# Kernel optimization log

Hardware: AMD Instinct MI355X
Metric: run time of the kernel (lower is better)

## Reference

```python
import jax, jax.numpy as jnp
import numpy as np
from jax import lax

EPS = 1e-10
BN_EPS = 1e-5
T = 0.1
K = 64
B, D, H, Z = 2048, 2048, 512, 500


def _bn(x, g, b):
    # training-mode BatchNorm1d: biased batch stats over axis 0
    mu = x.mean(axis=0)
    var = ((x - mu) ** 2).mean(axis=0)
    return g * (x - mu) / jnp.sqrt(var + BN_EPS) + b


def _leaky(x):
    return jnp.where(x >= 0, x, 0.01 * x)


def setup_inputs() -> dict:
    key = jax.random.key(0)
    ks = jax.random.split(key, 16)
    def lin(k, fan_in, shape):
        return jax.random.normal(k, shape, jnp.float32) / np.sqrt(fan_in)
    return {
        'x': jax.random.uniform(ks[0], (B, D), jnp.float32),
        'u_gumbel': jax.random.uniform(ks[1], (B, D), jnp.float32),
        'eps': jax.random.normal(ks[2], (B, Z), jnp.float32),
        'wc_w1': lin(ks[3], D, (D, H)), 'wc_b1': jnp.zeros((H,)),
        'wc_g': jnp.ones((H,)), 'wc_beta': jnp.zeros((H,)),
        'wc_w2': lin(ks[4], H, (H, D)), 'wc_b2': jnp.zeros((D,)),
        'enc_w1': lin(ks[5], D, (D, 2 * H)), 'enc_b1': jnp.zeros((2 * H,)),
        'enc_g1': jnp.ones((2 * H,)), 'enc_beta1': jnp.zeros((2 * H,)),
        'enc_w2': lin(ks[6], 2 * H, (2 * H, H)), 'enc_b2': jnp.zeros((H,)),
        'enc_g2': jnp.ones((H,)), 'enc_beta2': jnp.zeros((H,)),
        'enc_w3': lin(ks[7], H, (H, H)), 'enc_b3': jnp.zeros((H,)),
        'enc_g3': jnp.ones((H,)), 'enc_beta3': jnp.zeros((H,)),
        'fc21_w': lin(ks[8], H, (H, Z)), 'fc21_b': jnp.zeros((Z,)),
        'fc22_w': lin(ks[9], H, (H, Z)), 'fc22_b': jnp.zeros((Z,)),
        'fc3_w': lin(ks[10], Z, (Z, H)), 'fc3_b': jnp.zeros((H,)),
        'fc3_g': jnp.ones((H,)), 'fc3_beta': jnp.zeros((H,)),
        'fc4_w': lin(ks[11], H, (H, D)), 'fc4_b': jnp.zeros((D,)),
    }


def _sample_subset(w_logits, u):
    # gumbel_keys: w += log(-log(u')) with u' in (EPS, 1)
    u = (1.0 - EPS) * u + EPS
    w = w_logits + jnp.log(-jnp.log(u))

    def step(carry, _):
        w, onehot, acc = carry
        khot_mask = jnp.maximum(1.0 - onehot, EPS)
        w = w + jnp.log(khot_mask)
        onehot = jax.nn.softmax(w / T, axis=-1)
        return (w, onehot, acc + onehot), None

    init = (w, jnp.zeros_like(w), jnp.zeros_like(w))
    (_, _, khot), _ = lax.scan(step, init, None, length=K)
    return khot


def reference(x, u_gumbel, eps,
              wc_w1, wc_b1, wc_g, wc_beta, wc_w2, wc_b2,
              enc_w1, enc_b1, enc_g1, enc_beta1,
              enc_w2, enc_b2, enc_g2, enc_beta2,
              enc_w3, enc_b3, enc_g3, enc_beta3,
              fc21_w, fc21_b, fc22_w, fc22_b,
              fc3_w, fc3_b, fc3_g, fc3_beta, fc4_w, fc4_b):
    # weight_creator: Linear -> BN -> ReLU -> Linear
    h = jax.nn.relu(_bn(x @ wc_w1 + wc_b1, wc_g, wc_beta))
    w_logits = h @ wc_w2 + wc_b2
    khot = _sample_subset(w_logits, u_gumbel)  # [B, D]
    xm = x * khot
    h1 = _leaky(_bn(xm @ enc_w1 + enc_b1, enc_g1, enc_beta1))
    h1 = _leaky(_bn(h1 @ enc_w2 + enc_b2, enc_g2, enc_beta2))
    h1 = _leaky(_bn(h1 @ enc_w3 + enc_b3, enc_g3, enc_beta3))
    mu = h1 @ fc21_w + fc21_b
    logvar = h1 @ fc22_w + fc22_b
    z = mu + eps * jnp.exp(0.5 * logvar)
    hd = _leaky(_bn(z @ fc3_w + fc3_b, fc3_g, fc3_beta))
    mu_x = jax.nn.sigmoid(hd @ fc4_w + fc4_b)
    return (mu_x, mu, logvar)
```

## Files before the change

### kernel.cpp

```cpp
#include <hip/hip_runtime.h>
#include <hip/hip_bf16.h>
#include <math.h>

#define B_DIM 2048
#define D_DIM 2048
#define H_DIM 512
#define Z_DIM 500

#define ACT_NONE 0
#define ACT_RELU 1
#define ACT_SIGMOID 2
#define ACT_LEAKY 3

typedef __attribute__((ext_vector_type(8))) _Float16 f16x8;
typedef __attribute__((ext_vector_type(4))) _Float16 f16x4;
typedef __attribute__((ext_vector_type(4))) float f32x4;

template<int BM, int BN, int TERMS>
__global__ __launch_bounds__(256, 2) void gemm_f16(
    const _Float16* __restrict__ Ah_, const _Float16* __restrict__ Al_,
    const _Float16* __restrict__ Bh_, const _Float16* __restrict__ Bl_,
    const float* __restrict__ bias, float* __restrict__ C,
    float* __restrict__ part, int M, int N, int K, int act, int Kc)
{
    constexpr int LDK = 40;
    constexpr int NPL = (TERMS == 3) ? 2 : 1;
    constexpr int PSA = BM * LDK, PSB = BN * LDK;
    constexpr int BUF = NPL * (PSA + PSB);
    constexpr int MT = BM / 32, NT = BN / 32;
    constexpr int CA = BM / 64, CB = BN / 64;
    __shared__ _Float16 smem[2 * BUF];

    const int t = threadIdx.x, lane = t & 63, wv = t >> 6;
    const int wrow = wv >> 1, wcol = wv & 1;
    const int row0 = blockIdx.y * BM, col0 = blockIdx.x * BN;
    const int ks = blockIdx.z * Kc;
    const int nk = Kc >> 5;

    f16x8 rA[CA][NPL], rB[CB][NPL];

    auto gload = [&](int kt) {
        #pragma unroll
        for (int i = 0; i < CA; ++i) {
            int id = t + i * 256;
            int r = id >> 2, ko = (id & 3) * 8;
            size_t off = (size_t)(row0 + r) * K + kt + ko;
            rA[i][0] = *(const f16x8*)(Ah_ + off);
            if constexpr (TERMS == 3) rA[i][1] = *(const f16x8*)(Al_ + off);
        }
        #pragma unroll
        for (int i = 0; i < CB; ++i) {
            int id = t + i * 256;
            int r = id >> 2, ko = (id & 3) * 8;
            size_t off = (size_t)(col0 + r) * K + kt + ko;
            rB[i][0] = *(const f16x8*)(Bh_ + off);
            if constexpr (TERMS == 3) rB[i][1] = *(const f16x8*)(Bl_ + off);
        }
    };
    auto cstore = [&](int b) {
        _Float16* base = smem + b * BUF;
        #pragma unroll
        for (int i = 0; i < CA; ++i) {
            int id = t + i * 256;
            int r = id >> 2, ko = (id & 3) * 8;
            *(f16x8*)&base[r * LDK + ko] = rA[i][0];
            if constexpr (TERMS == 3) *(f16x8*)&base[PSA + r * LDK + ko] = rA[i][1];
        }
        _Float16* bb = base + NPL * PSA;
        #pragma unroll
        for (int i = 0; i < CB; ++i) {
            int id = t + i * 256;
            int r = id >> 2, ko = (id & 3) * 8;
            *(f16x8*)&bb[r * LDK + ko] = rB[i][0];
            if constexpr (TERMS == 3) *(f16x8*)&bb[PSB + r * LDK + ko] = rB[i][1];
        }
    };

    f32x4 acc[MT][NT];
    #pragma unroll
    for (int i = 0; i < MT; ++i)
        #pragma unroll
        for (int j = 0; j < NT; ++j) {
            f32x4 z = {0.f, 0.f, 0.f, 0.f};
            acc[i][j] = z;
        }

    const int q8 = (lane >> 4) * 8, fr = lane & 15;

    gload(ks);
    cstore(0);
    __syncthreads();

    for (int it = 0; it < nk; ++it) {
        int cur = it & 1;
        if (it + 1 < nk) gload(ks + (it + 1) * 32);

        const _Float16* A0 = smem + cur * BUF;
        const _Float16* A1 = A0 + PSA;
        const _Float16* B0 = A0 + NPL * PSA;
        const _Float16* B1 = B0 + PSB;
        f16x8 ah[MT], al[MT], bh[NT], bl[NT];
        #pragma unroll
        for (int i = 0; i < MT; ++i) {
            int r = wrow * (BM / 2) + i * 16 + fr;
            ah[i] = *(const f16x8*)&A0[r * LDK + q8];
            if constexpr (TERMS == 3) al[i] = *(const f16x8*)&A1[r * LDK + q8];
        }
        #pragma unroll
        for (int j = 0; j < NT; ++j) {
            int n = wcol * (BN / 2) + j * 16 + fr;
            bh[j] = *(const f16x8*)&B0[n * LDK + q8];
            if constexpr (TERMS == 3) bl[j] = *(const f16x8*)&B1[n * LDK + q8];
        }
        #pragma unroll
        for (int i = 0; i < MT; ++i)
            #pragma unroll
            for (int j = 0; j < NT; ++j) {
                acc[i][j] = __builtin_amdgcn_mfma_f32_16x16x32_f16(ah[i], bh[j], acc[i][j], 0, 0, 0);
                if constexpr (TERMS == 3) {
                    acc[i][j] = __builtin_amdgcn_mfma_f32_16x16x32_f16(ah[i], bl[j], acc[i][j], 0, 0, 0);
                    acc[i][j] = __builtin_amdgcn_mfma_f32_16x16x32_f16(al[i], bh[j], acc[i][j], 0, 0, 0);
                }
            }

        if (it + 1 < nk) cstore(cur ^ 1);
        __syncthreads();
    }

    const bool dopart = (gridDim.z > 1);
    float* dst = dopart ? (part + (size_t)blockIdx.z * M * N) : C;
    #pragma unroll
    for (int i = 0; i < MT; ++i) {
        int rbase = row0 + wrow * (BM / 2) + i * 16 + (lane >> 4) * 4;
        #pragma unroll
        for (int j = 0; j < NT; ++j) {
            int c = col0 + wcol * (BN / 2) + j * 16 + (lane & 15);
            if (c < N) {
                float b = dopart ? 0.f : bias[c];
                #pragma unroll
                for (int q = 0; q < 4; ++q) {
                    float v = acc[i][j][q] + b;
                    if (!dopart && act == ACT_SIGMOID)
                        v = 1.f / (1.f + __builtin_amdgcn_exp2f(-v * 1.44269504f));
                    dst[(size_t)(rbase + q) * N + c] = v;
                }
            }
        }
    }
}

__global__ __launch_bounds__(256) void cvt_split_x(
    const float* __restrict__ x, _Float16* __restrict__ xh,
    _Float16* __restrict__ xl, int n4)
{
    int i = blockIdx.x * 256 + threadIdx.x;
    if (i >= n4) return;
    float4 v = ((const float4*)x)[i];
    f16x4 h, l;
    h[0]=(_Float16)v.x; l[0]=(_Float16)(v.x-(float)h[0]);
    h[1]=(_Float16)v.y; l[1]=(_Float16)(v.y-(float)h[1]);
    h[2]=(_Float16)v.z; l[2]=(_Float16)(v.z-(float)h[2]);
    h[3]=(_Float16)v.w; l[3]=(_Float16)(v.w-(float)h[3]);
    ((f16x4*)xh)[i] = h;
    ((f16x4*)xl)[i] = l;
}

__global__ __launch_bounds__(256) void cvt_w_t(
    const float* __restrict__ in, _Float16* __restrict__ outh,
    _Float16* __restrict__ outl, int K, int N, int Kp)
{
    __shared__ float tile[32][33];
    const int t = threadIdx.x;
    const int tk0 = blockIdx.x * 32, tn0 = blockIdx.y * 32;
    const int lx = t & 31, ly = t >> 5;
    #pragma unroll
    for (int r = 0; r < 4; ++r) {
        int k = tk0 + ly + r * 8, n = tn0 + lx;
        tile[ly + r * 8][lx] = (k < K && n < N) ? in[(size_t)k * N + n] : 0.f;
    }
    __syncthreads();
    #pragma unroll
    for (int r = 0; r < 4; ++r) {
        int n = tn0 + ly + r * 8, k = tk0 + lx;
        float v = tile[lx][ly + r * 8];
        _Float16 h = (_Float16)v;
        outh[(size_t)n * Kp + k] = h;
        if (outl) outl[(size_t)n * Kp + k] = (_Float16)(v - (float)h);
    }
}

__global__ __launch_bounds__(256) void reduce_bias(
    const float* __restrict__ part, int S, int MN, int N,
    const float* __restrict__ bias, float* __restrict__ C, int act)
{
    int i = blockIdx.x * 256 + threadIdx.x;
    if (i >= MN) return;
    float s = bias[i % N];
    for (int k = 0; k < S; ++k) s += part[(size_t)k * MN + i];
    if (act == ACT_SIGMOID) s = 1.f / (1.f + __builtin_amdgcn_exp2f(-s * 1.44269504f));
    C[i] = s;
}

__global__ __launch_bounds__(256) void colstats_partial(
    const float* __restrict__ Y, float* __restrict__ part,
    int Brows, int N, int rowsPerBlock)
{
    const int t = threadIdx.x;
    const int col = blockIdx.x * 64 + (t & 63);
    const int g = blockIdx.y;
    const int r0 = g * rowsPerBlock;
    const int r1 = min(r0 + rowsPerBlock, Brows);
    float s = 0.f, s2 = 0.f;
    for (int r = r0 + (t >> 6); r < r1; r += 4) {
        float v = Y[(size_t)r * N + col];
        s += v;
        s2 += v * v;
    }
    __shared__ float ss[4][64], ss2[4][64];
    ss[t >> 6][t & 63] = s;
    ss2[t >> 6][t & 63] = s2;
    __syncthreads();
    if (t < 64) {
        s  = ss[0][t] + ss[1][t] + ss[2][t] + ss[3][t];
        s2 = ss2[0][t] + ss2[1][t] + ss2[2][t] + ss2[3][t];
        float* p = part + ((size_t)g * N + col) * 2;
        p[0] = s;
        p[1] = s2;
    }
}

__global__ __launch_bounds__(256) void colstats_final(
    const float* __restrict__ part, int G, int N, int Brows,
    const float* __restrict__ gamma, const float* __restrict__ beta,
    float* __restrict__ scale, float* __restrict__ shift)
{
    int c = blockIdx.x * 256 + threadIdx.x;
    if (c >= N) return;
    float s = 0.f, s2 = 0.f;
    for (int g = 0; g < G; ++g) {
        s  += part[((size_t)g * N + c) * 2];
        s2 += part[((size_t)g * N + c) * 2 + 1];
    }
    float invB = 1.f / (float)Brows;
    float mean = s * invB;
    float var  = s2 * invB - mean * mean;
    float rstd = rsqrtf(var + 1e-5f);
    float sc = gamma[c] * rstd;
    scale[c] = sc;
    shift[c] = beta[c] - mean * sc;
}

__global__ __launch_bounds__(256) void bn_apply_f16(
    const float* __restrict__ Y, const float* __restrict__ scale,
    const float* __restrict__ shift, _Float16* __restrict__ oh,
    _Float16* __restrict__ ol, int total, int N, int act)
{
    int idx = blockIdx.x * 256 + threadIdx.x;
    int i4 = idx * 4;
    if (i4 >= total) return;
    float4 y = *(const float4*)(Y + i4);
    int c = i4 % N;
    float4 sc = *(const float4*)(scale + c);
    float4 sh = *(const float4*)(shift + c);
    float r[4];
    r[0] = y.x * sc.x + sh.x;
    r[1] = y.y * sc.y + sh.y;
    r[2] = y.z * sc.z + sh.z;
    r[3] = y.w * sc.w + sh.w;
    #pragma unroll
    for (int q = 0; q < 4; ++q) {
        if (act == ACT_RELU) r[q] = fmaxf(r[q], 0.f);
        else if (act == ACT_LEAKY) r[q] = (r[q] >= 0.f) ? r[q] : 0.01f * r[q];
    }
    f16x4 h;
    #pragma unroll
    for (int q = 0; q < 4; ++q) h[q] = (_Float16)r[q];
    ((f16x4*)oh)[idx] = h;
    if (ol) {
        f16x4 l;
        #pragma unroll
        for (int q = 0; q < 4; ++q) l[q] = (_Float16)(r[q] - (float)h[q]);
        ((f16x4*)ol)[idx] = l;
    }
}

__global__ __launch_bounds__(256) void gumbel_scan(
    const float* __restrict__ WLg, const float* __restrict__ U,
    const float* __restrict__ X, _Float16* __restrict__ XM)
{
    const int row = blockIdx.x;
    const int t = threadIdx.x, wv = t >> 6, lane = t & 63;
    const float* wrow = WLg + (size_t)row * D_DIM;
    const float* urow = U + (size_t)row * D_DIM;
    const float* xrow = X + (size_t)row * D_DIM;
    _Float16* xmrow = XM + (size_t)row * D_DIM;

    const float L2E = 1.4426950408889634f;
    const float LOG2LN2 = -0.5287663729448977f;

    __shared__ float sW[2][4], sS[2][4];

    float W[8], e[8], acc[8];
    #pragma unroll
    for (int j = 0; j < 8; ++j) {
        int c = t + j * 256;
        float u = fmaf(urow[c], 1.0f - 1e-10f, 1e-10f);
        float tl = -__builtin_amdgcn_logf(u);
        float w2 = fmaf(wrow[c], L2E, __builtin_amdgcn_logf(tl) + LOG2LN2);
        W[j] = __builtin_amdgcn_exp2f(w2);
        e[j] = 0.f;
        acc[j] = 0.f;
    }
    float inv = 0.f;

    for (int it = 0; it < 64; ++it) {
        const int p = it & 1;
        float lm = 0.f;
        #pragma unroll
        for (int j = 0; j < 8; ++j) {
            acc[j] = fmaf(e[j], inv, acc[j]);
            float msk = fmaxf(fmaf(-e[j], inv, 1.0f), 1e-10f);
            W[j] *= msk;
            lm = fmaxf(lm, W[j]);
        }
        #pragma unroll
        for (int off = 32; off; off >>= 1)
            lm = fmaxf(lm, __shfl_xor(lm, off));
        if (lane == 0) sW[p][wv] = lm;
        __syncthreads();
        float Wm = fmaxf(fmaxf(sW[p][0], sW[p][1]), fmaxf(sW[p][2], sW[p][3]));
        float rm = 1.0f / Wm;
        float s = 0.f;
        #pragma unroll
        for (int j = 0; j < 8; ++j) {
            float r1 = W[j] * rm;
            float r2 = r1 * r1;
            float r4 = r2 * r2;
            float r5 = r4 * r1;
            float ee = r5 * r5;
            e[j] = ee;
            s += ee;
        }
        #pragma unroll
        for (int off = 32; off; off >>= 1)
            s += __shfl_xor(s, off);
        if (lane == 0) sS[p][wv] = s;
        __syncthreads();
        s = (sS[p][0] + sS[p][1]) + (sS[p][2] + sS[p][3]);
        inv = 1.0f / s;
    }

    #pragma unroll
    for (int j = 0; j < 8; ++j) {
        int c = t + j * 256;
        float a = fmaf(e[j], inv, acc[j]);
        xmrow[c] = (_Float16)(xrow[c] * a);
    }
}

__global__ __launch_bounds__(256) void z_kernel16(
    const float* __restrict__ mu, const float* __restrict__ lv,
    const float* __restrict__ eps, _Float16* __restrict__ zb, int n4)
{
    int i = blockIdx.x * 256 + threadIdx.x;
    if (i >= n4) return;
    int f = i * 4;
    int row = f / Z_DIM, col = f - row * Z_DIM;
    float4 m = *(const float4*)(mu + f);
    float4 l = *(const float4*)(lv + f);
    float4 e = *(const float4*)(eps + f);
    const float HL2E = 0.7213475204444817f;
    f16x4 r;
    r[0] = (_Float16)(m.x + e.x * __builtin_amdgcn_exp2f(l.x * HL2E));
    r[1] = (_Float16)(m.y + e.y * __builtin_amdgcn_exp2f(l.y * HL2E));
    r[2] = (_Float16)(m.z + e.z * __builtin_amdgcn_exp2f(l.z * HL2E));
    r[3] = (_Float16)(m.w + e.w * __builtin_amdgcn_exp2f(l.w * HL2E));
    *(f16x4*)(zb + (size_t)row * 512 + col) = r;
}

extern "C" void kernel_launch(void* const* d_in, const int* in_sizes, int n_in,
                              void* d_out, int out_size, void* d_ws, size_t ws_size,
                              hipStream_t stream) {
    const float* x        = (const float*)d_in[0];
    const float* u_gumbel = (const float*)d_in[1];
    const float* eps      = (const float*)d_in[2];
    const float* wc_w1    = (const float*)d_in[3];
    const float* wc_b1    = (const float*)d_in[4];
    const float* wc_g     = (const float*)d_in[5];
    const float* wc_beta  = (const float*)d_in[6];
    const float* wc_w2    = (const float*)d_in[7];
    const float* wc_b2    = (const float*)d_in[8];
    const float* enc_w1   = (const float*)d_in[9];
    const float* enc_b1   = (const float*)d_in[10];
    const float* enc_g1   = (const float*)d_in[11];
    const float* enc_beta1= (const float*)d_in[12];
    const float* enc_w2   = (const float*)d_in[13];
    const float* enc_b2   = (const float*)d_in[14];
    const float* enc_g2   = (const float*)d_in[15];
    const float* enc_beta2= (const float*)d_in[16];
    const float* enc_w3   = (const float*)d_in[17];
    const float* enc_b3   = (const float*)d_in[18];
    const float* enc_g3   = (const float*)d_in[19];
    const float* enc_beta3= (const float*)d_in[20];
    const float* fc21_w   = (const float*)d_in[21];
    const float* fc21_b   = (const float*)d_in[22];
    const float* fc22_w   = (const float*)d_in[23];
    const float* fc22_b   = (const float*)d_in[24];
    const float* fc3_w    = (const float*)d_in[25];
    const float* fc3_b    = (const float*)d_in[26];
    const float* fc3_g    = (const float*)d_in[27];
    const float* fc3_beta = (const float*)d_in[28];
    const float* fc4_w    = (const float*)d_in[29];
    const float* fc4_b    = (const float*)d_in[30];

    float* out   = (float*)d_out;
    float* mu_x  = out;
    float* mu    = out + (size_t)B_DIM * D_DIM;
    float* lv    = mu + (size_t)B_DIM * Z_DIM;

    const size_t F1M = 1u << 20;
    float* wsf = (float*)d_ws;
    float*     P_WL  = wsf;
    _Float16*  xh    = (_Float16*)(wsf + 4 * F1M);
    _Float16*  xl    = (_Float16*)(wsf + 6 * F1M);
    _Float16*  xm16  = (_Float16*)(wsf + 4 * F1M);
    float*     Yb    = wsf + 6 * F1M;
    _Float16*  a2    = (_Float16*)(wsf + 8 * F1M);
    _Float16*  a3    = (_Float16*)(wsf + 9 * F1M);
    _Float16*  a4    = (_Float16*)(wsf + 9 * F1M + F1M / 2);
    _Float16*  zb16  = (_Float16*)(wsf + 10 * F1M);
    _Float16*  a5    = (_Float16*)(wsf + 10 * F1M + F1M / 2);
    float*     Hbuf  = wsf + 11 * F1M;
    _Float16*  Hh    = (_Float16*)(wsf + 12 * F1M);
    _Float16*  Hl    = (_Float16*)(wsf + 12 * F1M + F1M / 2);
    _Float16*  w1th  = (_Float16*)(wsf + 13 * F1M);
    _Float16*  w1tl  = (_Float16*)(wsf + 13 * F1M + F1M / 2);
    _Float16*  w2th  = (_Float16*)(wsf + 14 * F1M);
    _Float16*  w2tl  = (_Float16*)(wsf + 14 * F1M + F1M / 2);
    _Float16*  e1t   = (_Float16*)(wsf + 15 * F1M);
    _Float16*  e2t   = (_Float16*)(wsf + 16 * F1M);
    _Float16*  e3t   = (_Float16*)(wsf + 16 * F1M + F1M / 4);
    _Float16*  f21t  = (_Float16*)(wsf + 16 * F1M + 3 * (F1M / 8));
    _Float16*  f22t  = (_Float16*)(wsf + 16 * F1M + 4 * (F1M / 8));
    _Float16*  f3t   = (_Float16*)(wsf + 16 * F1M + 5 * (F1M / 8));
    _Float16*  f4t   = (_Float16*)(wsf + 16 * F1M + 6 * (F1M / 8));
    float*     bnp   = wsf + 17 * F1M + F1M / 4;
    float*     scale = bnp + 16384;
    float*     shift = scale + 2048;

    const int G = 8;

    auto gemm3 = [&](const _Float16* Ah, const _Float16* Al,
                     const _Float16* Bh, const _Float16* Bl,
                     const float* b, float* C, float* part,
                     int N, int K, int SK) {
        dim3 grid((N + 63) / 64, B_DIM / 128, SK);
        gemm_f16<128, 64, 3><<<grid, 256, 0, stream>>>(Ah, Al, Bh, Bl, b, C, part,
                                                       B_DIM, N, K, ACT_NONE, K / SK);
    };
    auto gemm1 = [&](const _Float16* Ah, const _Float16* Bh,
                     const float* b, float* C, float* part,
                     int N, int K, int act, int SK) {
        dim3 grid((N + 63) / 64, B_DIM / 128, SK);
        gemm_f16<128, 64, 1><<<grid, 256, 0, stream>>>(Ah, nullptr, Bh, nullptr, b, C,
                                                       part, B_DIM, N, K, act, K / SK);
    };
    auto reduceK = [&](const float* part, int S, int N, const float* b, float* C) {
        int MN = B_DIM * N;
        reduce_bias<<<(MN + 255) / 256, 256, 0, stream>>>(part, S, MN, N, b, C, ACT_NONE);
    };
    auto bn = [&](const float* Y, const float* g_, const float* b_,
                  _Float16* oh, _Float16* ol, int N, int act) {
        dim3 gp(N / 64, G);
        colstats_partial<<<gp, 256, 0, stream>>>(Y, bnp, B_DIM, N, B_DIM / G);
        colstats_final<<<(N + 255) / 256, 256, 0, stream>>>(bnp, G, N, B_DIM, g_, b_, scale, shift);
        int total = B_DIM * N;
        bn_apply_f16<<<(total / 4 + 255) / 256, 256, 0, stream>>>(Y, scale, shift, oh, ol, total, N, act);
    };
    auto cvtw = [&](const float* in, _Float16* oh, _Float16* ol, int K, int N, int Kp, int Np) {
        dim3 grid(Kp / 32, Np / 32);
        cvt_w_t<<<grid, 256, 0, stream>>>(in, oh, ol, K, N, Kp);
    };

    cvt_split_x<<<4096, 256, 0, stream>>>(x, xh, xl, B_DIM * D_DIM / 4);
    cvtw(wc_w1, w1th, w1tl, 2048, 512, 2048, 512);
    cvtw(wc_w2, w2th, w2tl, 512, 2048, 512, 2048);
    cvtw(enc_w1, e1t, nullptr, 2048, 1024, 2048, 1024);
    cvtw(enc_w2, e2t, nullptr, 1024, 512, 1024, 512);
    cvtw(enc_w3, e3t, nullptr, 512, 512, 512, 512);
    cvtw(fc21_w, f21t, nullptr, 512, 500, 512, 512);
    cvtw(fc22_w, f22t, nullptr, 512, 500, 512, 512);
    cvtw(fc3_w, f3t, nullptr, 500, 512, 512, 512);
    cvtw(fc4_w, f4t, nullptr, 512, 2048, 512, 2048);

    gemm3(xh, xl, w1th, w1tl, nullptr, nullptr, P_WL, 512, 2048, 4);
    reduceK(P_WL, 4, 512, wc_b1, Hbuf);
    bn(Hbuf, wc_g, wc_beta, Hh, Hl, 512, ACT_RELU);
    gemm3(Hh, Hl, w2th, w2tl, wc_b2, P_WL, nullptr, 2048, 512, 1);

    gumbel_scan<<<B_DIM, 256, 0, stream>>>(P_WL, u_gumbel, x, xm16);

    gemm1(xm16, e1t, nullptr, nullptr, P_WL, 1024, 2048, ACT_NONE, 2);
    reduceK(P_WL, 2, 1024, enc_b1, Yb);
    bn(Yb, enc_g1, enc_beta1, a2, nullptr, 1024, ACT_LEAKY);
    gemm1(a2, e2t, nullptr, nullptr, P_WL, 512, 1024, ACT_NONE, 4);
    reduceK(P_WL, 4, 512, enc_b2, Yb);
    bn(Yb, enc_g2, enc_beta2, a3, nullptr, 512, ACT_LEAKY);
    gemm1(a3, e3t, nullptr, nullptr, P_WL, 512, 512, ACT_NONE, 4);
    reduceK(P_WL, 4, 512, enc_b3, Yb);
    bn(Yb, enc_g3, enc_beta3, a4, nullptr, 512, ACT_LEAKY);

    gemm1(a4, f21t, nullptr, nullptr, P_WL, 500, 512, ACT_NONE, 4);
    reduceK(P_WL, 4, 500, fc21_b, mu);
    gemm1(a4, f22t, nullptr, nullptr, P_WL, 500, 512, ACT_NONE, 4);
    reduceK(P_WL, 4, 500, fc22_b, lv);

    hipMemsetAsync(zb16, 0, (size_t)B_DIM * 512 * sizeof(_Float16), stream);
    int n4 = B_DIM * Z_DIM / 4;
    z_kernel16<<<(n4 + 255) / 256, 256, 0, stream>>>(mu, lv, eps, zb16, n4);

    gemm1(zb16, f3t, nullptr, nullptr, P_WL, 512, 512, ACT_NONE, 4);
    reduceK(P_WL, 4, 512, fc3_b, Yb);
    bn(Yb, fc3_g, fc3_beta, a5, nullptr, 512, ACT_LEAKY);
    gemm1(a5, f4t, fc4_b, mu_x, nullptr, 2048, 512, ACT_SIGMOID, 1);
}
```

Before: 465.2 us.

## Merge gumbel scan reductions into one barrier per iteration using stale max

The 64-step softmax scan in gumbel_scan now runs one combined max+sum block reduction per iteration instead of two. It normalises by the previous iteration's max, which is valid because the mask only ever shrinks W, so the ratio stays at or below one. The loop also uses packed f32x2 arithmetic, hardware rcp, and vectorised 8-wide loads and stores per thread. The cost is that the exponent is computed against a stale max, so there is a small underflow or precision risk, and the initial max needs an extra reduction.

```diff
diff --git a/kernel.cpp b/kernel.cpp
--- a/kernel.cpp
+++ b/kernel.cpp
@@ -15,6 +15,7 @@
 typedef __attribute__((ext_vector_type(8))) _Float16 f16x8;
 typedef __attribute__((ext_vector_type(4))) _Float16 f16x4;
 typedef __attribute__((ext_vector_type(4))) float f32x4;
+typedef __attribute__((ext_vector_type(2))) float f32x2;
 
 template<int BM, int BN, int TERMS>
 __global__ __launch_bounds__(256, 2) void gemm_f16(
@@ -290,71 +291,111 @@
 {
     const int row = blockIdx.x;
     const int t = threadIdx.x, wv = t >> 6, lane = t & 63;
-    const float* wrow = WLg + (size_t)row * D_DIM;
-    const float* urow = U + (size_t)row * D_DIM;
-    const float* xrow = X + (size_t)row * D_DIM;
-    _Float16* xmrow = XM + (size_t)row * D_DIM;
+    const float* wrow = WLg + (size_t)row * D_DIM + 8 * t;
+    const float* urow = U + (size_t)row * D_DIM + 8 * t;
+    const float* xrow = X + (size_t)row * D_DIM + 8 * t;
+    _Float16* xmrow = XM + (size_t)row * D_DIM + 8 * t;
 
     const float L2E = 1.4426950408889634f;
     const float LOG2LN2 = -0.5287663729448977f;
 
-    __shared__ float sW[2][4], sS[2][4];
-
-    float W[8], e[8], acc[8];
-    #pragma unroll
-    for (int j = 0; j < 8; ++j) {
-        int c = t + j * 256;
-        float u = fmaf(urow[c], 1.0f - 1e-10f, 1e-10f);
+    __shared__ f32x2 sLS[2][4];
+    __shared__ float sM0[4];
+
+    f32x2 W2[4], e2[4], acc2[4];
+
+    auto mkW = [&](float wl, float uu) -> float {
+        float u = fmaf(uu, 1.0f - 1e-10f, 1e-10f);
         float tl = -__builtin_amdgcn_logf(u);
-        float w2 = fmaf(wrow[c], L2E, __builtin_amdgcn_logf(tl) + LOG2LN2);
-        W[j] = __builtin_amdgcn_exp2f(w2);
-        e[j] = 0.f;
-        acc[j] = 0.f;
-    }
+        return __builtin_amdgcn_exp2f(fmaf(wl, L2E, __builtin_amdgcn_logf(tl) + LOG2LN2));
+    };
+
+    {
+        float4 ua = *(const float4*)urow, ub = *(const float4*)(urow + 4);
+        float4 wa = *(const float4*)wrow, wb = *(const float4*)(wrow + 4);
+        W2[0] = f32x2{mkW(wa.x, ua.x), mkW(wa.y, ua.y)};
+        W2[1] = f32x2{mkW(wa.z, ua.z), mkW(wa.w, ua.w)};
+        W2[2] = f32x2{mkW(wb.x, ub.x), mkW(wb.y, ub.y)};
+        W2[3] = f32x2{mkW(wb.z, ub.z), mkW(wb.w, ub.w)};
+    }
+    #pragma unroll
+    for (int j = 0; j < 4; ++j) {
+        e2[j] = f32x2{0.f, 0.f};
+        acc2[j] = f32x2{0.f, 0.f};
+    }
+
+    float m;
+    {
+        f32x2 lv = f32x2{0.f, 0.f};
+        #pragma unroll
+        for (int j = 0; j < 4; ++j) {
+            lv.x = fmaxf(lv.x, W2[j].x);
+            lv.y = fmaxf(lv.y, W2[j].y);
+        }
+        float lm = fmaxf(lv.x, lv.y);
+        #pragma unroll
+        for (int off = 32; off; off >>= 1)
+            lm = fmaxf(lm, __shfl_xor(lm, off));
+        if (lane == 0) sM0[wv] = lm;
+        __syncthreads();
+        m = fmaxf(fmaxf(sM0[0], sM0[1]), fmaxf(sM0[2], sM0[3]));
+    }
+
     float inv = 0.f;
-
     for (int it = 0; it < 64; ++it) {
         const int p = it & 1;
-        float lm = 0.f;
-        #pragma unroll
-        for (int j = 0; j < 8; ++j) {
-            acc[j] = fmaf(e[j], inv, acc[j]);
-            float msk = fmaxf(fmaf(-e[j], inv, 1.0f), 1e-10f);
-            W[j] *= msk;
-            lm = fmaxf(lm, W[j]);
-        }
-        #pragma unroll
-        for (int off = 32; off; off >>= 1)
+        const float rm = __builtin_amdgcn_rcpf(m);
+        f32x2 lmv = f32x2{0.f, 0.f}, sv = f32x2{0.f, 0.f};
+        #pragma unroll
+        for (int j = 0; j < 4; ++j) {
+            f32x2 oh = e2[j] * inv;
+            acc2[j] += oh;
+            f32x2 msk = 1.0f - oh;
+            msk.x = fmaxf(msk.x, 1e-10f);
+            msk.y = fmaxf(msk.y, 1e-10f);
+            f32x2 Wn = W2[j] * msk;
+            W2[j] = Wn;
+            f32x2 r = Wn * rm;
+            f32x2 q2 = r * r;
+            f32x2 q4 = q2 * q2;
+            f32x2 q8 = q4 * q4;
+            f32x2 ee = q8 * q2;
+            e2[j] = ee;
+            sv += ee;
+            lmv.x = fmaxf(lmv.x, Wn.x);
+            lmv.y = fmaxf(lmv.y, Wn.y);
+        }
+        float lm = fmaxf(lmv.x, lmv.y);
+        float s = sv.x + sv.y;
+        #pragma unroll
+        for (int off = 32; off; off >>= 1) {
             lm = fmaxf(lm, __shfl_xor(lm, off));
-        if (lane == 0) sW[p][wv] = lm;
+            s += __shfl_xor(s, off);
+        }
+        if (lane == 0) sLS[p][wv] = f32x2{lm, s};
         __syncthreads();
-        float Wm = fmaxf(fmaxf(sW[p][0], sW[p][1]), fmaxf(sW[p][2], sW[p][3]));
-        float rm = 1.0f / Wm;
-        float s = 0.f;
-        #pragma unroll
-        for (int j = 0; j < 8; ++j) {
-            float r1 = W[j] * rm;
-            float r2 = r1 * r1;
-            float r4 = r2 * r2;
-            float r5 = r4 * r1;
-            float ee = r5 * r5;
-            e[j] = ee;
-            s += ee;
-        }
-        #pragma unroll
-        for (int off = 32; off; off >>= 1)
-            s += __shfl_xor(s, off);
-        if (lane == 0) sS[p][wv] = s;
-        __syncthreads();
-        s = (sS[p][0] + sS[p][1]) + (sS[p][2] + sS[p][3]);
-        inv = 1.0f / s;
-    }
-
-    #pragma unroll
-    for (int j = 0; j < 8; ++j) {
-        int c = t + j * 256;
-        float a = fmaf(e[j], inv, acc[j]);
-        xmrow[c] = (_Float16)(xrow[c] * a);
+        f32x2 r0 = sLS[p][0], r1 = sLS[p][1], r2 = sLS[p][2], r3 = sLS[p][3];
+        m = fmaxf(fmaxf(r0.x, r1.x), fmaxf(r2.x, r3.x));
+        float st = (r0.y + r1.y) + (r2.y + r3.y);
+        inv = __builtin_amdgcn_rcpf(st);
+    }
+
+    {
+        float4 xa = *(const float4*)xrow, xb = *(const float4*)(xrow + 4);
+        f32x2 a0 = acc2[0] + e2[0] * inv;
+        f32x2 a1 = acc2[1] + e2[1] * inv;
+        f32x2 a2 = acc2[2] + e2[2] * inv;
+        f32x2 a3 = acc2[3] + e2[3] * inv;
+        f16x8 o;
+        o[0] = (_Float16)(xa.x * a0.x);
+        o[1] = (_Float16)(xa.y * a0.y);
+        o[2] = (_Float16)(xa.z * a1.x);
+        o[3] = (_Float16)(xa.w * a1.y);
+        o[4] = (_Float16)(xb.x * a2.x);
+        o[5] = (_Float16)(xb.y * a2.y);
+        o[6] = (_Float16)(xb.z * a3.x);
+        o[7] = (_Float16)(xb.w * a3.y);
+        *(f16x8*)xmrow = o;
     }
 }
 
```

Result: faster. 455.4 us (-2.1%).

## Fuse split-K reduce into BN stats and make gumbel scan one row per wave

Applied to the files above, without the earlier changes.

Replaces the separate split-K reduce_bias plus colstats_partial pair with a single reduce_stats kernel that sums partials, adds bias, writes Y and accumulates column stats, using 64 row groups instead of 8. Rewrites gumbel_scan so each wavefront owns a full row (32 elements per lane, vectorised loads and stores), which removes the block-level __syncthreads and shared-memory reductions. The per-step max renormalisation now refreshes only every 4 iterations, with the other steps reusing a stale max. This trades exact per-step max scaling for fewer reductions, with some overflow or precision risk in the x^10 power, and uses more registers per thread.

```diff
diff --git a/kernel.cpp b/kernel.cpp
--- a/kernel.cpp
+++ b/kernel.cpp
@@ -15,6 +15,10 @@
 typedef __attribute__((ext_vector_type(8))) _Float16 f16x8;
 typedef __attribute__((ext_vector_type(4))) _Float16 f16x4;
 typedef __attribute__((ext_vector_type(4))) float f32x4;
+
+__device__ __forceinline__ float rfl(float x) {
+    return __uint_as_float(__builtin_amdgcn_readfirstlane(__float_as_uint(x)));
+}
 
 template<int BM, int BN, int TERMS>
 __global__ __launch_bounds__(256, 2) void gemm_f16(
@@ -201,18 +205,23 @@
     C[i] = s;
 }
 
-__global__ __launch_bounds__(256) void colstats_partial(
-    const float* __restrict__ Y, float* __restrict__ part,
-    int Brows, int N, int rowsPerBlock)
+__global__ __launch_bounds__(256) void reduce_stats(
+    const float* __restrict__ part, int S, int Brows, int N, int rowsPerBlock,
+    const float* __restrict__ bias, float* __restrict__ Y,
+    float* __restrict__ statp)
 {
     const int t = threadIdx.x;
     const int col = blockIdx.x * 64 + (t & 63);
     const int g = blockIdx.y;
     const int r0 = g * rowsPerBlock;
     const int r1 = min(r0 + rowsPerBlock, Brows);
+    const size_t MN = (size_t)Brows * N;
+    const float b = bias[col];
     float s = 0.f, s2 = 0.f;
     for (int r = r0 + (t >> 6); r < r1; r += 4) {
-        float v = Y[(size_t)r * N + col];
+        float v = b;
+        for (int k = 0; k < S; ++k) v += part[k * MN + (size_t)r * N + col];
+        Y[(size_t)r * N + col] = v;
         s += v;
         s2 += v * v;
     }
@@ -223,7 +232,7 @@
     if (t < 64) {
         s  = ss[0][t] + ss[1][t] + ss[2][t] + ss[3][t];
         s2 = ss2[0][t] + ss2[1][t] + ss2[2][t] + ss2[3][t];
-        float* p = part + ((size_t)g * N + col) * 2;
+        float* p = statp + ((size_t)g * N + col) * 2;
         p[0] = s;
         p[1] = s2;
     }
@@ -288,8 +297,8 @@
     const float* __restrict__ WLg, const float* __restrict__ U,
     const float* __restrict__ X, _Float16* __restrict__ XM)
 {
-    const int row = blockIdx.x;
-    const int t = threadIdx.x, wv = t >> 6, lane = t & 63;
+    const int wv = threadIdx.x >> 6, lane = threadIdx.x & 63;
+    const int row = blockIdx.x * 4 + wv;
     const float* wrow = WLg + (size_t)row * D_DIM;
     const float* urow = U + (size_t)row * D_DIM;
     const float* xrow = X + (size_t)row * D_DIM;
@@ -298,63 +307,80 @@
     const float L2E = 1.4426950408889634f;
     const float LOG2LN2 = -0.5287663729448977f;
 
-    __shared__ float sW[2][4], sS[2][4];
-
-    float W[8], e[8], acc[8];
+    float W[32], acc[32];
+
+    auto mkW = [&](float wl, float uu) -> float {
+        float u = fmaf(uu, 1.0f - 1e-10f, 1e-10f);
+        float tl = -__builtin_amdgcn_logf(u);
+        return __builtin_amdgcn_exp2f(fmaf(wl, L2E, __builtin_amdgcn_logf(tl) + LOG2LN2));
+    };
+
     #pragma unroll
     for (int j = 0; j < 8; ++j) {
-        int c = t + j * 256;
-        float u = fmaf(urow[c], 1.0f - 1e-10f, 1e-10f);
-        float tl = -__builtin_amdgcn_logf(u);
-        float w2 = fmaf(wrow[c], L2E, __builtin_amdgcn_logf(tl) + LOG2LN2);
-        W[j] = __builtin_amdgcn_exp2f(w2);
-        e[j] = 0.f;
-        acc[j] = 0.f;
-    }
-    float inv = 0.f;
+        float4 u4 = *(const float4*)(urow + j * 256 + lane * 4);
+        float4 w4 = *(const float4*)(wrow + j * 256 + lane * 4);
+        W[4*j  ] = mkW(w4.x, u4.x);
+        W[4*j+1] = mkW(w4.y, u4.y);
+        W[4*j+2] = mkW(w4.z, u4.z);
+        W[4*j+3] = mkW(w4.w, u4.w);
+        acc[4*j] = 0.f; acc[4*j+1] = 0.f; acc[4*j+2] = 0.f; acc[4*j+3] = 0.f;
+    }
+
+    float rm_s;
+    {
+        float lm = 0.f;
+        #pragma unroll
+        for (int j = 0; j < 32; ++j) lm = fmaxf(lm, W[j]);
+        #pragma unroll
+        for (int off = 32; off; off >>= 1)
+            lm = fmaxf(lm, __shfl_xor(lm, off));
+        rm_s = rfl(__builtin_amdgcn_rcpf(lm));
+    }
 
     for (int it = 0; it < 64; ++it) {
-        const int p = it & 1;
+        float e[32];
+        float s = 0.f;
+        #pragma unroll
+        for (int j = 0; j < 32; ++j) {
+            float r1 = W[j] * rm_s;
+            float q2 = r1 * r1;
+            float q4 = q2 * q2;
+            float q8 = q4 * q4;
+            float ee = q8 * q2;
+            e[j] = ee;
+            s += ee;
+        }
+        #pragma unroll
+        for (int off = 32; off; off >>= 1)
+            s += __shfl_xor(s, off);
+        float inv = rfl(__builtin_amdgcn_rcpf(s));
+
+        const bool refresh = ((it & 3) == 3);
         float lm = 0.f;
         #pragma unroll
-        for (int j = 0; j < 8; ++j) {
+        for (int j = 0; j < 32; ++j) {
             acc[j] = fmaf(e[j], inv, acc[j]);
             float msk = fmaxf(fmaf(-e[j], inv, 1.0f), 1e-10f);
             W[j] *= msk;
-            lm = fmaxf(lm, W[j]);
-        }
-        #pragma unroll
-        for (int off = 32; off; off >>= 1)
-            lm = fmaxf(lm, __shfl_xor(lm, off));
-        if (lane == 0) sW[p][wv] = lm;
-        __syncthreads();
-        float Wm = fmaxf(fmaxf(sW[p][0], sW[p][1]), fmaxf(sW[p][2], sW[p][3]));
-        float rm = 1.0f / Wm;
-        float s = 0.f;
-        #pragma unroll
-        for (int j = 0; j < 8; ++j) {
-            float r1 = W[j] * rm;
-            float r2 = r1 * r1;
-            float r4 = r2 * r2;
-            float r5 = r4 * r1;
-            float ee = r5 * r5;
-            e[j] = ee;
-            s += ee;
-        }
-        #pragma unroll
-        for (int off = 32; off; off >>= 1)
-            s += __shfl_xor(s, off);
-        if (lane == 0) sS[p][wv] = s;
-        __syncthreads();
-        s = (sS[p][0] + sS[p][1]) + (sS[p][2] + sS[p][3]);
-        inv = 1.0f / s;
+            if (refresh) lm = fmaxf(lm, W[j]);
+        }
+        if (refresh) {
+            #pragma unroll
+            for (int off = 32; off; off >>= 1)
+                lm = fmaxf(lm, __shfl_xor(lm, off));
+            rm_s = rfl(__builtin_amdgcn_rcpf(lm));
+        }
     }
 
     #pragma unroll
     for (int j = 0; j < 8; ++j) {
-        int c = t + j * 256;
-        float a = fmaf(e[j], inv, acc[j]);
-        xmrow[c] = (_Float16)(xrow[c] * a);
+        float4 x4 = *(const float4*)(xrow + j * 256 + lane * 4);
+        f16x4 o;
+        o[0] = (_Float16)(x4.x * acc[4*j  ]);
+        o[1] = (_Float16)(x4.y * acc[4*j+1]);
+        o[2] = (_Float16)(x4.z * acc[4*j+2]);
+        o[3] = (_Float16)(x4.w * acc[4*j+3]);
+        *(f16x4*)(xmrow + j * 256 + lane * 4) = o;
     }
 }
 
@@ -445,10 +471,10 @@
     _Float16*  f3t   = (_Float16*)(wsf + 16 * F1M + 5 * (F1M / 8));
     _Float16*  f4t   = (_Float16*)(wsf + 16 * F1M + 6 * (F1M / 8));
     float*     bnp   = wsf + 17 * F1M + F1M / 4;
-    float*     scale = bnp + 16384;
+    float*     scale = bnp + 131072;
     float*     shift = scale + 2048;
 
-    const int G = 8;
+    const int G = 64;
 
     auto gemm3 = [&](const _Float16* Ah, const _Float16* Al,
                      const _Float16* Bh, const _Float16* Bl,
@@ -469,11 +495,12 @@
         int MN = B_DIM * N;
         reduce_bias<<<(MN + 255) / 256, 256, 0, stream>>>(part, S, MN, N, b, C, ACT_NONE);
     };
-    auto bn = [&](const float* Y, const float* g_, const float* b_,
-                  _Float16* oh, _Float16* ol, int N, int act) {
+    auto bnFromParts = [&](const float* part, int S, const float* b,
+                           const float* g_, const float* beta_,
+                           float* Y, _Float16* oh, _Float16* ol, int N, int act) {
         dim3 gp(N / 64, G);
-        colstats_partial<<<gp, 256, 0, stream>>>(Y, bnp, B_DIM, N, B_DIM / G);
-        colstats_final<<<(N + 255) / 256, 256, 0, stream>>>(bnp, G, N, B_DIM, g_, b_, scale, shift);
+        reduce_stats<<<gp, 256, 0, stream>>>(part, S, B_DIM, N, B_DIM / G, b, Y, bnp);
+        colstats_final<<<(N + 255) / 256, 256, 0, stream>>>(bnp, G, N, B_DIM, g_, beta_, scale, shift);
         int total = B_DIM * N;
         bn_apply_f16<<<(total / 4 + 255) / 256, 256, 0, stream>>>(Y, scale, shift, oh, ol, total, N, act);
     };
@@ -494,21 +521,17 @@
     cvtw(fc4_w, f4t, nullptr, 512, 2048, 512, 2048);
 
     gemm3(xh, xl, w1th, w1tl, nullptr, nullptr, P_WL, 512, 2048, 4);
-    reduceK(P_WL, 4, 512, wc_b1, Hbuf);
-    bn(Hbuf, wc_g, wc_beta, Hh, Hl, 512, ACT_RELU);
+    bnFromParts(P_WL, 4, wc_b1, wc_g, wc_beta, Hbuf, Hh, Hl, 512, ACT_RELU);
     gemm3(Hh, Hl, w2th, w2tl, wc_b2, P_WL, nullptr, 2048, 512, 1);
 
-    gumbel_scan<<<B_DIM, 256, 0, stream>>>(P_WL, u_gumbel, x, xm16);
+    gumbel_scan<<<B_DIM / 4, 256, 0, stream>>>(P_WL, u_gumbel, x, xm16);
 
     gemm1(xm16, e1t, nullptr, nullptr, P_WL, 1024, 2048, ACT_NONE, 2);
-    reduceK(P_WL, 2, 1024, enc_b1, Yb);
-    bn(Yb, enc_g1, enc_beta1, a2, nullptr, 1024, ACT_LEAKY);
+    bnFromParts(P_WL, 2, enc_b1, enc_g1, enc_beta1, Yb, a2, nullptr, 1024, ACT_LEAKY);
     gemm1(a2, e2t, nullptr, nullptr, P_WL, 512, 1024, ACT_NONE, 4);
-    reduceK(P_WL, 4, 512, enc_b2, Yb);
-    bn(Yb, enc_g2, enc_beta2, a3, nullptr, 512, ACT_LEAKY);
+    bnFromParts(P_WL, 4, enc_b2, enc_g2, enc_beta2, Yb, a3, nullptr, 512, ACT_LEAKY);
     gemm1(a3, e3t, nullptr, nullptr, P_WL, 512, 512, ACT_NONE, 4);
-    reduceK(P_WL, 4, 512, enc_b3, Yb);
-    bn(Yb, enc_g3, enc_beta3, a4, nullptr, 512, ACT_LEAKY);
+    bnFromParts(P_WL, 4, enc_b3, enc_g3, enc_beta3, Yb, a4, nullptr, 512, ACT_LEAKY);
 
     gemm1(a4, f21t, nullptr, nullptr, P_WL, 500, 512, ACT_NONE, 4);
     reduceK(P_WL, 4, 500, fc21_b, mu);
@@ -520,7 +543,6 @@
     z_kernel16<<<(n4 + 255) / 256, 256, 0, stream>>>(mu, lv, eps, zb16, n4);
 
     gemm1(zb16, f3t, nullptr, nullptr, P_WL, 512, 512, ACT_NONE, 4);
-    reduceK(P_WL, 4, 512, fc3_b, Yb);
-    bn(Yb, fc3_g, fc3_beta, a5, nullptr, 512, ACT_LEAKY);
+    bnFromParts(P_WL, 4, fc3_b, fc3_g, fc3_beta, Yb, a5, nullptr, 512, ACT_LEAKY);
     gemm1(a5, f4t, fc4_b, mu_x, nullptr, 2048, 512, ACT_SIGMOID, 1);
 }
```

New measurement: 445.0 us. -4.3%, faster.
